# Kernel optimization log

Hardware: AMD Instinct MI355X
Metric: run time of the kernel (lower is better)

## Reference

```python
import jax, jax.numpy as jnp
import numpy as np
from jax import lax

DILATIONS = [2 ** i for i in range(9)] * 5  # 45 layers
RD, SD, QD, KF = 32, 512, 256, 33  # residual, skip, quantization channels, causal kernel
PAD = int(np.sum(DILATIONS)) + KF // 2  # 2571
L_IN = 165142  # finallen = L_IN - 2*PAD = 160000


def conv1d(x, w, b, d=1):
    # x: [N, Cin, L], w: [Cout, Cin, K] -> [N, Cout, L - d*(K-1)] (VALID)
    y = lax.conv_general_dilated(x, w, window_strides=(1,), padding='VALID',
                                 rhs_dilation=(d,),
                                 dimension_numbers=('NCH', 'OIH', 'NCH'))
    return y + b[None, :, None]


def setup_inputs() -> dict:
    key = jax.random.key(0)
    ks = jax.random.split(key, 16)
    f = lambda k, s: jax.random.normal(k, s, dtype=jnp.float32) * 0.1
    return {
        'x': jax.random.normal(ks[0], (1, 1, L_IN), dtype=jnp.float32),
        'w_causal': f(ks[1], (RD, 1, KF)), 'b_causal': f(ks[2], (RD,)),
        'w_tanh': f(ks[3], (45, RD, RD, 3)), 'b_tanh': f(ks[4], (45, RD)),
        'w_sig': f(ks[5], (45, RD, RD, 3)), 'b_sig': f(ks[6], (45, RD)),
        'w_skip': f(ks[7], (45, SD, RD, 1)), 'b_skip': f(ks[8], (45, SD)),
        'w_dense': f(ks[9], (45, RD, RD, 1)), 'b_dense': f(ks[10], (45, RD)),
        'w_post1': f(ks[11], (SD, SD, 1)), 'b_post1': f(ks[12], (SD,)),
        'w_post2': f(ks[13], (QD, SD, 1)), 'b_post2': f(ks[14], (QD,)),
    }


def reference(x, w_causal, b_causal, w_tanh, b_tanh, w_sig, b_sig,
              w_skip, b_skip, w_dense, b_dense,
              w_post1, b_post1, w_post2, b_post2):
    finallen = x.shape[-1] - 2 * PAD  # static
    x = conv1d(x, w_causal, b_causal)  # [1, RD, L-32]
    skip = jnp.zeros((1, SD, finallen), dtype=jnp.float32)
    for i, d in enumerate(DILATIONS):  # fixed 45-layer stack
        xin = x[:, :, d:-d]  # residual path, matches VALID dilated conv output length
        x1 = jnp.tanh(conv1d(x, w_tanh[i], b_tanh[i], d))
        x2 = jax.nn.sigmoid(conv1d(x, w_sig[i], b_sig[i], d))
        x = x1 * x2
        cut = (x.shape[-1] - finallen) // 2  # static
        s = conv1d(x, w_skip[i], b_skip[i])  # [1, SD, cur_len]
        skip = skip + s[:, :, cut:cut + finallen]
        x = conv1d(x, w_dense[i], b_dense[i]) + xin
    h = jax.nn.relu(conv1d(jax.nn.relu(skip), w_post1, b_post1))
    return conv1d(h, w_post2, b_post2)  # [1, QD, finallen]
```

## Files before the change

kernel.cpp:

```cpp
#include <hip/hip_runtime.h>
#include <hip/hip_bf16.h>
#include <cstdio>

typedef unsigned short ushort_t;
typedef __bf16 bf16x8 __attribute__((ext_vector_type(8)));
typedef float f32x4 __attribute__((ext_vector_type(4)));

#define FL   160000
#define L0   165110
#define NL   45
#define CH   80000

__device__ __forceinline__ float tanh_fast(float x) {
    float ax = fabsf(x);
    float e  = __expf(-2.f * ax);
    float r  = (1.f - e) / (1.f + e);
    return copysignf(r, x);
}
__device__ __forceinline__ float sigmoid_fast(float x) {
    return 1.f / (1.f + __expf(-x));
}

#define GLOAD_LDS16(gp, lp) \
    __builtin_amdgcn_global_load_lds( \
        (const __attribute__((address_space(1))) void*)(gp), \
        (__attribute__((address_space(3))) void*)(lp), 16, 0, 0)

__global__ __launch_bounds__(256) void causal_kernel(
    const float* __restrict__ x, const float* __restrict__ wc,
    const float* __restrict__ bc, float* __restrict__ y)
{
    __shared__ float ws_[33 * 32];
    __shared__ float bs_[32];
    const int tid = threadIdx.x;
    for (int idx = tid; idx < 33 * 32; idx += 256) {
        int k = idx >> 5, oc = idx & 31;
        ws_[idx] = wc[oc * 33 + k];
    }
    if (tid < 32) bs_[tid] = bc[tid];
    __syncthreads();
    const int t = blockIdx.x * 256 + tid;
    if (t >= L0) return;
    float acc[32];
#pragma unroll
    for (int oc = 0; oc < 32; ++oc) acc[oc] = bs_[oc];
    for (int k = 0; k < 33; ++k) {
        float xv = x[t + k];
        const float* wp = &ws_[k * 32];
#pragma unroll
        for (int oc = 0; oc < 32; ++oc) acc[oc] += wp[oc] * xv;
    }
    float* yr = y + (size_t)t * 32;
#pragma unroll
    for (int oc = 0; oc < 32; oc += 4)
        *(float4*)(yr + oc) = make_float4(acc[oc], acc[oc+1], acc[oc+2], acc[oc+3]);
}

__global__ __launch_bounds__(256) void prepack_frag(
    const float* __restrict__ wt, const float* __restrict__ wsg,
    const float* __restrict__ wd,
    __bf16* __restrict__ fragConv, __bf16* __restrict__ fragDense)
{
    const int idx = blockIdx.x * 256 + threadIdx.x;
    if (idx < NL * 12 * 64) {
        const int lane = idx & 63;
        const int rem  = idx >> 6;
        const int slot = rem % 12, l = rem / 12;
        const int j = slot >> 2, i = slot & 3;
        const int m = (i & 1) * 16 + (lane & 15);
        const int quad = lane >> 4;
        const float* wsrc = (i < 2) ? wt : wsg;
        __bf16 v[8];
#pragma unroll
        for (int jj = 0; jj < 8; ++jj) {
            int ic = quad * 8 + jj;
            v[jj] = (__bf16)wsrc[((size_t)(l * 32 + m) * 32 + ic) * 3 + j];
        }
        *(uint4*)(fragConv + (size_t)idx * 8) = *(const uint4*)v;
    }
    if (idx < NL * 2 * 64) {
        const int lane = idx & 63;
        const int rem  = idx >> 6;
        const int i = rem & 1, l = rem >> 1;
        const int m = i * 16 + (lane & 15);
        const int quad = lane >> 4;
        __bf16 v[8];
#pragma unroll
        for (int jj = 0; jj < 8; ++jj)
            v[jj] = (__bf16)wd[(size_t)(l * 32 + m) * 32 + quad * 8 + jj];
        *(uint4*)(fragDense + (size_t)idx * 8) = *(const uint4*)v;
    }
}

__global__ __launch_bounds__(256) void layer_mfma(
    const float* __restrict__ xin,
    float* __restrict__ xout,
    __bf16* __restrict__ xslot,
    const __bf16* __restrict__ fragConv,
    const __bf16* __restrict__ fragDense,
    const float* __restrict__ bt, const float* __restrict__ bs,
    const float* __restrict__ bd,
    int d, int Lout, int S)
{
    __shared__ __bf16 gbuf[4][32][40];
    const int tid  = threadIdx.x;
    const int wave = tid >> 6, lane = tid & 63;
    const int fm = lane & 15, quad = lane >> 4;
    const int t0 = blockIdx.x * 128 + wave * 32;

    bf16x8 Ac[3][4], Ad[2];
#pragma unroll
    for (int j = 0; j < 3; ++j)
#pragma unroll
        for (int i = 0; i < 4; ++i)
            Ac[j][i] = *(const bf16x8*)(fragConv + ((j * 4 + i) * 64 + lane) * 8);
#pragma unroll
    for (int i = 0; i < 2; ++i)
        Ad[i] = *(const bf16x8*)(fragDense + (i * 64 + lane) * 8);

    f32x4 acc[4][2];
#pragma unroll
    for (int i = 0; i < 4; ++i) {
        const float* bb = (i < 2) ? (bt + i * 16) : (bs + (i - 2) * 16);
        float4 b4 = *(const float4*)(bb + quad * 4);
        f32x4 bi; bi[0] = b4.x; bi[1] = b4.y; bi[2] = b4.z; bi[3] = b4.w;
        acc[i][0] = bi; acc[i][1] = bi;
    }

#pragma unroll
    for (int j2 = 0; j2 < 2; ++j2) {
        int tl = t0 + j2 * 16 + fm;
        if (tl > Lout - 1) tl = Lout - 1;
#pragma unroll
        for (int j = 0; j < 3; ++j) {
            const float* xp = xin + (size_t)(tl + j * d) * 32 + quad * 8;
            float4 u0 = *(const float4*)xp;
            float4 u1 = *(const float4*)(xp + 4);
            bf16x8 bf;
            bf[0] = (__bf16)u0.x; bf[1] = (__bf16)u0.y;
            bf[2] = (__bf16)u0.z; bf[3] = (__bf16)u0.w;
            bf[4] = (__bf16)u1.x; bf[5] = (__bf16)u1.y;
            bf[6] = (__bf16)u1.z; bf[7] = (__bf16)u1.w;
#pragma unroll
            for (int i = 0; i < 4; ++i)
                acc[i][j2] = __builtin_amdgcn_mfma_f32_16x16x32_bf16(
                    Ac[j][i], bf, acc[i][j2], 0, 0, 0);
        }
    }

#pragma unroll
    for (int i = 0; i < 2; ++i)
#pragma unroll
        for (int j2 = 0; j2 < 2; ++j2) {
            __bf16 pk[4];
#pragma unroll
            for (int r = 0; r < 4; ++r)
                pk[r] = (__bf16)(tanh_fast(acc[i][j2][r]) *
                                 sigmoid_fast(acc[i + 2][j2][r]));
            *(uint2*)&gbuf[wave][j2 * 16 + fm][i * 16 + quad * 4] =
                *(const uint2*)pk;
        }

    {
        const int rr = lane >> 1, hh = lane & 1;
        const int t = t0 + rr, tw = t - S;
        if (t < Lout && (unsigned)tw < FL) {
            const char* gp = (const char*)&gbuf[wave][rr][0] + hh * 32;
            uint4 v0 = *(const uint4*)gp;
            uint4 v1 = *(const uint4*)(gp + 16);
            uint4* dst = (uint4*)(xslot + (size_t)tw * 1440 + hh * 16);
            dst[0] = v0; dst[1] = v1;
        }
    }

    f32x4 dacc[2][2];
#pragma unroll
    for (int i = 0; i < 2; ++i) {
        float4 b4 = *(const float4*)(bd + i * 16 + quad * 4);
        f32x4 bi; bi[0] = b4.x; bi[1] = b4.y; bi[2] = b4.z; bi[3] = b4.w;
        dacc[i][0] = bi; dacc[i][1] = bi;
    }
#pragma unroll
    for (int j2 = 0; j2 < 2; ++j2) {
        bf16x8 gb = *(const bf16x8*)&gbuf[wave][j2 * 16 + fm][quad * 8];
#pragma unroll
        for (int i = 0; i < 2; ++i)
            dacc[i][j2] = __builtin_amdgcn_mfma_f32_16x16x32_bf16(
                Ad[i], gb, dacc[i][j2], 0, 0, 0);
    }
#pragma unroll
    for (int i = 0; i < 2; ++i)
#pragma unroll
        for (int j2 = 0; j2 < 2; ++j2) {
            const int t = t0 + j2 * 16 + fm;
            if (t < Lout) {
                const int oc = i * 16 + quad * 4;
                float4 r4 = *(const float4*)(xin + (size_t)(t + d) * 32 + oc);
                float4 o;
                o.x = dacc[i][j2][0] + r4.x;
                o.y = dacc[i][j2][1] + r4.y;
                o.z = dacc[i][j2][2] + r4.z;
                o.w = dacc[i][j2][3] + r4.w;
                *(float4*)(xout + (size_t)t * 32 + oc) = o;
            }
        }
}

template<bool TSTORE>
__global__ __launch_bounds__(512, 2) void gemm256(
    const __bf16* __restrict__ A, int lda,
    const __bf16* __restrict__ Bt, int ldb,
    void* __restrict__ Cout, int ldc,
    const float* __restrict__ bias, int K, int Ncur, int mTile)
{
    __shared__ __bf16 lds[4 * 16384];
    const int tid  = threadIdx.x;
    const int wave = tid >> 6, lane = tid & 63;
    const int fm = lane & 15, quad = lane >> 4;
    const int wm = wave >> 2, wn = wave & 3;

    const int nwg = gridDim.x;
    const int q8 = nwg >> 3, r8 = nwg & 7;
    const int xcd = blockIdx.x & 7, loc = blockIdx.x >> 3;
    const int sbid = (xcd < r8 ? xcd * (q8 + 1)
                               : r8 * (q8 + 1) + (xcd - r8) * q8) + loc;
    const int m0 = (sbid % mTile) * 256;
    const int n0 = (sbid / mTile) * 256;

    const __bf16* pS[4];
    int dstE[4];
#pragma unroll
    for (int i = 0; i < 4; ++i) {
        const int cidx = (i & 1) * 512 + tid;
        const int r = cidx >> 2, c = cidx & 3;
        const int cs = c ^ ((r >> 1) & 3);
        if (i < 2) {
            pS[i] = A + (size_t)(m0 + r) * lda + cs * 8;
        } else {
            int rg = n0 + r; if (rg > Ncur - 1) rg = Ncur - 1;
            pS[i] = Bt + (size_t)rg * ldb + cs * 8;
        }
        dstE[i] = ((i < 2) ? 0 : 8192) + (i & 1) * 4096 + wave * 512;
    }

    const int swz = ((quad ^ ((fm >> 1) & 3)) << 3);
    const int aoff = (wm * 128 + fm) * 32 + swz;
    const int boff = 8192 + (wn * 64 + fm) * 32 + swz;

    f32x4 acc[8][4] = {};

    auto do_stage = [&](int t) {
        const int pb = (t & 3) * 16384;
        const int ko = t * 32;
#pragma unroll
        for (int i = 0; i < 4; ++i)
            GLOAD_LDS16(pS[i] + ko, lds + pb + dstE[i]);
    };
    auto tile_compute = [&](int t) {
        const int pb = (t & 3) * 16384;
        bf16x8 af[8], bg[4];
#pragma unroll
        for (int i = 0; i < 8; ++i)
            af[i] = *(const bf16x8*)(lds + pb + aoff + i * 512);
#pragma unroll
        for (int j = 0; j < 4; ++j)
            bg[j] = *(const bf16x8*)(lds + pb + boff + j * 512);
        __builtin_amdgcn_s_setprio(1);
#pragma unroll
        for (int i = 0; i < 8; ++i)
#pragma unroll
            for (int j = 0; j < 4; ++j)
                acc[i][j] = __builtin_amdgcn_mfma_f32_16x16x32_bf16(
                    af[i], bg[j], acc[i][j], 0, 0, 0);
        __builtin_amdgcn_s_setprio(0);
    };

    const int NT = K >> 5;
    do_stage(0); do_stage(1); do_stage(2);
    for (int t = 0; t < NT - 3; ++t) {
        asm volatile("s_waitcnt vmcnt(8)" ::: "memory");
        __builtin_amdgcn_s_barrier();
        __builtin_amdgcn_sched_barrier(0);
        do_stage(t + 3);
        tile_compute(t);
    }
    asm volatile("s_waitcnt vmcnt(8)" ::: "memory");
    __builtin_amdgcn_s_barrier();
    __builtin_amdgcn_sched_barrier(0);
    tile_compute(NT - 3);
    asm volatile("s_waitcnt vmcnt(4)" ::: "memory");
    __builtin_amdgcn_s_barrier();
    __builtin_amdgcn_sched_barrier(0);
    tile_compute(NT - 2);
    asm volatile("s_waitcnt vmcnt(0)" ::: "memory");
    __builtin_amdgcn_s_barrier();
    __builtin_amdgcn_sched_barrier(0);
    tile_compute(NT - 1);

    if (TSTORE) {
        __bf16* O = (__bf16*)Cout;
#pragma unroll
        for (int i = 0; i < 8; ++i) {
            const int m = m0 + wm * 128 + i * 16 + quad * 4;
            const float4 bv = *(const float4*)(bias + m);
#pragma unroll
            for (int j = 0; j < 4; ++j) {
                const int n = n0 + wn * 64 + j * 16 + fm;
                if (n < Ncur) {
                    __bf16 pk[4];
                    pk[0] = (__bf16)fmaxf(acc[i][j][0] + bv.x, 0.f);
                    pk[1] = (__bf16)fmaxf(acc[i][j][1] + bv.y, 0.f);
                    pk[2] = (__bf16)fmaxf(acc[i][j][2] + bv.z, 0.f);
                    pk[3] = (__bf16)fmaxf(acc[i][j][3] + bv.w, 0.f);
                    *(uint2*)(O + (size_t)n * ldc + m) = *(const uint2*)pk;
                }
            }
        }
    } else {
        float* O = (float*)Cout;
#pragma unroll
        for (int i = 0; i < 8; ++i) {
            const int m = m0 + wm * 128 + i * 16 + quad * 4;
            const float4 bv = *(const float4*)(bias + m);
#pragma unroll
            for (int j = 0; j < 4; ++j) {
                const int n = n0 + wn * 64 + j * 16 + fm;
                if (n < Ncur) {
                    O[(size_t)(m + 0) * ldc + n] = acc[i][j][0] + bv.x;
                    O[(size_t)(m + 1) * ldc + n] = acc[i][j][1] + bv.y;
                    O[(size_t)(m + 2) * ldc + n] = acc[i][j][2] + bv.z;
                    O[(size_t)(m + 3) * ldc + n] = acc[i][j][3] + bv.w;
                }
            }
        }
    }
}

__global__ __launch_bounds__(256) void repack_kernel(
    const float* __restrict__ wskip, const float* __restrict__ bskip,
    __bf16* __restrict__ wcat, float* __restrict__ bsum)
{
    const int idx = blockIdx.x * 256 + threadIdx.x;
    if (idx < 512 * 1440) {
        int oc = idx / 1440, lic = idx % 1440;
        int l = lic >> 5, ic = lic & 31;
        wcat[idx] = (__bf16)wskip[((size_t)l * 512 + oc) * 32 + ic];
    }
    if (idx < 512) {
        float s = 0.f;
        for (int l = 0; l < NL; ++l) s += bskip[l * 512 + idx];
        bsum[idx] = s;
    }
}

__global__ __launch_bounds__(256) void repack_post(
    const float* __restrict__ w1, const float* __restrict__ w2,
    __bf16* __restrict__ wp1, __bf16* __restrict__ wp2)
{
    const int idx = blockIdx.x * 256 + threadIdx.x;
    if (idx < 512 * 512) wp1[idx] = (__bf16)w1[idx];
    if (idx < 256 * 512) wp2[idx] = (__bf16)w2[idx];
}

extern "C" void kernel_launch(void* const* d_in, const int* in_sizes, int n_in,
                              void* d_out, int out_size, void* d_ws, size_t ws_size,
                              hipStream_t stream)
{
    const float* x        = (const float*)d_in[0];
    const float* w_causal = (const float*)d_in[1];
    const float* b_causal = (const float*)d_in[2];
    const float* w_tanh   = (const float*)d_in[3];
    const float* b_tanh   = (const float*)d_in[4];
    const float* w_sig    = (const float*)d_in[5];
    const float* b_sig    = (const float*)d_in[6];
    const float* w_skip   = (const float*)d_in[7];
    const float* b_skip   = (const float*)d_in[8];
    const float* w_dense  = (const float*)d_in[9];
    const float* b_dense  = (const float*)d_in[10];
    const float* w_post1  = (const float*)d_in[11];
    const float* b_post1  = (const float*)d_in[12];
    const float* w_post2  = (const float*)d_in[13];
    const float* b_post2  = (const float*)d_in[14];
    float* out = (float*)d_out;

    char* base = (char*)d_ws;
    __bf16* XcatT  = (__bf16*)base;
    __bf16* skipTc = (__bf16*)(base + 460800000);
    __bf16* hTc    = (__bf16*)(base + 542720000);
    __bf16* wcat   = (__bf16*)(base + 624640000);
    __bf16* wp1    = (__bf16*)(base + 626114560);
    __bf16* wp2    = (__bf16*)(base + 626638848);
    float*  bsum   = (float*)(base + 626900992);
    __bf16* fragConv  = (__bf16*)(base + 626903040);
    __bf16* fragDense = (__bf16*)(base + 627456000);
    float*  xb0    = (float*)(base + 460800000);
    float*  xb1    = (float*)(base + 460800000 + 21135360);
    const size_t need = 627548160;
    if (ws_size < need) {
        fprintf(stderr, "kernel_launch: ws_size %zu < needed %zu\n", ws_size, need);
        return;
    }

    repack_kernel<<<2880, 256, 0, stream>>>(w_skip, b_skip, wcat, bsum);
    repack_post<<<1024, 256, 0, stream>>>(w_post1, w_post2, wp1, wp2);
    prepack_frag<<<(NL * 12 * 64 + 255) / 256, 256, 0, stream>>>(
        w_tanh, w_sig, w_dense, fragConv, fragDense);
    causal_kernel<<<(L0 + 255) / 256, 256, 0, stream>>>(x, w_causal, b_causal, xb0);

    int Lin = L0;
    int S   = 2555;
    float* xc = xb0;
    float* xn = xb1;
    for (int l = 0; l < NL; ++l) {
        const int d = 1 << (l % 9);
        const int Lout = Lin - 2 * d;
        S -= d;
        layer_mfma<<<(Lout + 127) / 128, 256, 0, stream>>>(
            xc, xn, XcatT + l * 32,
            fragConv + (size_t)l * 12 * 64 * 8,
            fragDense + (size_t)l * 2 * 64 * 8,
            b_tanh + l * 32, b_sig + l * 32, b_dense + l * 32,
            d, Lout, S);
        float* tmp = xc; xc = xn; xn = tmp;
        Lin = Lout;
    }

    const int nTile = (CH + 255) / 256;
    for (int c = 0; c < 2; ++c) {
        const int c0 = c * CH;
        gemm256<true><<<nTile * 2, 512, 0, stream>>>(
            wcat, 1440, XcatT + (size_t)c0 * 1440, 1440,
            skipTc, 512, bsum, 1440, CH, 2);
        gemm256<true><<<nTile * 2, 512, 0, stream>>>(
            wp1, 512, skipTc, 512, hTc, 512, b_post1, 512, CH, 2);
        gemm256<false><<<nTile, 512, 0, stream>>>(
            wp2, 512, hTc, 512, out + c0, FL, b_post2, 512, CH, 1);
    }
}
```

Measured before the change: 1.780 ms.

## Store per-layer gated activations in planar layout instead of interleaved concat

Each layer now writes its 32-channel gated output into its own contiguous [t][32] plane, instead of a 64-byte slot inside a 1440-wide row that interleaves all 45 layers. The skip GEMM takes separate k-tile strides for A and B so it walks layer planes directly, and the skip weights are repacked as a plain bf16 copy in [layer][oc][ic] order. The goal is contiguous, coalesced global writes in the layer kernel and contiguous row reads in the skip GEMM, in place of 64-byte accesses at a 2880-byte stride. The cost is a slightly more general GEMM address calculation using size_t strides.

```diff
diff --git a/kernel.cpp b/kernel.cpp
--- a/kernel.cpp
+++ b/kernel.cpp
@@ -168,7 +168,7 @@
             const char* gp = (const char*)&gbuf[wave][rr][0] + hh * 32;
             uint4 v0 = *(const uint4*)gp;
             uint4 v1 = *(const uint4*)(gp + 16);
-            uint4* dst = (uint4*)(xslot + (size_t)tw * 1440 + hh * 16);
+            uint4* dst = (uint4*)(xslot + (size_t)tw * 32 + hh * 16);
             dst[0] = v0; dst[1] = v1;
         }
     }
@@ -208,10 +208,10 @@
 
 template<bool TSTORE>
 __global__ __launch_bounds__(512, 2) void gemm256(
-    const __bf16* __restrict__ A, int lda,
-    const __bf16* __restrict__ Bt, int ldb,
+    const __bf16* __restrict__ A, const __bf16* __restrict__ Bt,
     void* __restrict__ Cout, int ldc,
-    const float* __restrict__ bias, int K, int Ncur, int mTile)
+    const float* __restrict__ bias, int K, int Ncur, int mTile,
+    int ldRow, size_t kStrA, size_t kStrB)
 {
     __shared__ __bf16 lds[4 * 16384];
     const int tid  = threadIdx.x;
@@ -235,10 +235,10 @@
         const int r = cidx >> 2, c = cidx & 3;
         const int cs = c ^ ((r >> 1) & 3);
         if (i < 2) {
-            pS[i] = A + (size_t)(m0 + r) * lda + cs * 8;
+            pS[i] = A + (size_t)(m0 + r) * ldRow + cs * 8;
         } else {
             int rg = n0 + r; if (rg > Ncur - 1) rg = Ncur - 1;
-            pS[i] = Bt + (size_t)rg * ldb + cs * 8;
+            pS[i] = Bt + (size_t)rg * ldRow + cs * 8;
         }
         dstE[i] = ((i < 2) ? 0 : 8192) + (i & 1) * 4096 + wave * 512;
     }
@@ -251,10 +251,12 @@
 
     auto do_stage = [&](int t) {
         const int pb = (t & 3) * 16384;
-        const int ko = t * 32;
-#pragma unroll
-        for (int i = 0; i < 4; ++i)
-            GLOAD_LDS16(pS[i] + ko, lds + pb + dstE[i]);
+        const size_t ka = (size_t)t * kStrA;
+        const size_t kb = (size_t)t * kStrB;
+        GLOAD_LDS16(pS[0] + ka, lds + pb + dstE[0]);
+        GLOAD_LDS16(pS[1] + ka, lds + pb + dstE[1]);
+        GLOAD_LDS16(pS[2] + kb, lds + pb + dstE[2]);
+        GLOAD_LDS16(pS[3] + kb, lds + pb + dstE[3]);
     };
     auto tile_compute = [&](int t) {
         const int pb = (t & 3) * 16384;
@@ -341,11 +343,7 @@
     __bf16* __restrict__ wcat, float* __restrict__ bsum)
 {
     const int idx = blockIdx.x * 256 + threadIdx.x;
-    if (idx < 512 * 1440) {
-        int oc = idx / 1440, lic = idx % 1440;
-        int l = lic >> 5, ic = lic & 31;
-        wcat[idx] = (__bf16)wskip[((size_t)l * 512 + oc) * 32 + ic];
-    }
+    if (idx < NL * 512 * 32) wcat[idx] = (__bf16)wskip[idx];
     if (idx < 512) {
         float s = 0.f;
         for (int l = 0; l < NL; ++l) s += bskip[l * 512 + idx];
@@ -384,10 +382,10 @@
     float* out = (float*)d_out;
 
     char* base = (char*)d_ws;
-    __bf16* XcatT  = (__bf16*)base;
+    __bf16* XcatT2 = (__bf16*)base;
     __bf16* skipTc = (__bf16*)(base + 460800000);
     __bf16* hTc    = (__bf16*)(base + 542720000);
-    __bf16* wcat   = (__bf16*)(base + 624640000);
+    __bf16* wcat2  = (__bf16*)(base + 624640000);
     __bf16* wp1    = (__bf16*)(base + 626114560);
     __bf16* wp2    = (__bf16*)(base + 626638848);
     float*  bsum   = (float*)(base + 626900992);
@@ -401,7 +399,7 @@
         return;
     }
 
-    repack_kernel<<<2880, 256, 0, stream>>>(w_skip, b_skip, wcat, bsum);
+    repack_kernel<<<2880, 256, 0, stream>>>(w_skip, b_skip, wcat2, bsum);
     repack_post<<<1024, 256, 0, stream>>>(w_post1, w_post2, wp1, wp2);
     prepack_frag<<<(NL * 12 * 64 + 255) / 256, 256, 0, stream>>>(
         w_tanh, w_sig, w_dense, fragConv, fragDense);
@@ -416,7 +414,7 @@
         const int Lout = Lin - 2 * d;
         S -= d;
         layer_mfma<<<(Lout + 127) / 128, 256, 0, stream>>>(
-            xc, xn, XcatT + l * 32,
+            xc, xn, XcatT2 + (size_t)l * FL * 32,
             fragConv + (size_t)l * 12 * 64 * 8,
             fragDense + (size_t)l * 2 * 64 * 8,
             b_tanh + l * 32, b_sig + l * 32, b_dense + l * 32,
@@ -429,11 +427,11 @@
     for (int c = 0; c < 2; ++c) {
         const int c0 = c * CH;
         gemm256<true><<<nTile * 2, 512, 0, stream>>>(
-            wcat, 1440, XcatT + (size_t)c0 * 1440, 1440,
-            skipTc, 512, bsum, 1440, CH, 2);
+            wcat2, XcatT2 + (size_t)c0 * 32, skipTc, 512, bsum,
+            1440, CH, 2, 32, (size_t)512 * 32, (size_t)FL * 32);
         gemm256<true><<<nTile * 2, 512, 0, stream>>>(
-            wp1, 512, skipTc, 512, hTc, 512, b_post1, 512, CH, 2);
+            wp1, skipTc, hTc, 512, b_post1, 512, CH, 2, 512, 32, 32);
         gemm256<false><<<nTile, 512, 0, stream>>>(
-            wp2, 512, hTc, 512, out + c0, FL, b_post2, 512, CH, 1);
-    }
-}
+            wp2, hTc, out + c0, FL, b_post2, 512, CH, 1, 512, 32, 32);
+    }
+}
```

Measured after the change: 1.580 ms. 11.2% less time.
